# Performance work log

Measured on AMD Instinct MI355X. Metric: run time of the kernel, lower is better.

## Reference

```python
import jax, jax.numpy as jnp
from jax import lax
import numpy as np

CH = 16
STAGES = 6
DN = ('NDHWC', 'DHWIO', 'NDHWC')


def setup_inputs() -> dict:
    key = jax.random.key(0)
    ks = jax.random.split(key, 16)
    B, G = 8, 64
    x = jax.random.normal(ks[0], (B, G, G, G, 1), dtype=jnp.float32)
    mask = jax.random.randint(ks[1], (B, G, G, G), 0, 2, dtype=jnp.int32)
    meta = jax.random.normal(ks[2], (B, 3), dtype=jnp.float32)
    sched = jax.random.normal(ks[3], (B, 128), dtype=jnp.float32)
    s = 0.05
    w_stem = jax.random.normal(ks[4], (5, 5, 5, 1, CH), dtype=jnp.float32) * s
    w_stages = jax.random.normal(ks[5], (STAGES, 3, 3, 3, CH, CH), dtype=jnp.float32) * s
    meta_w1 = jax.random.normal(ks[6], (3, 32), dtype=jnp.float32) * s
    meta_b1 = jnp.zeros((32,), jnp.float32)
    meta_w2 = jax.random.normal(ks[7], (32, 16), dtype=jnp.float32) * s
    meta_b2 = jnp.zeros((16,), jnp.float32)
    mat_w = jax.random.normal(ks[8], (CH * STAGES + 16, 128), dtype=jnp.float32) * s
    mat_b = jnp.zeros((128,), jnp.float32)
    sch_w = jax.random.normal(ks[9], (128, 128), dtype=jnp.float32) * s
    sch_b = jnp.zeros((128,), jnp.float32)
    f1_w = jax.random.normal(ks[10], (256, 128), dtype=jnp.float32) * s
    f1_b = jnp.zeros((128,), jnp.float32)
    f2_w = jax.random.normal(ks[11], (128, 1), dtype=jnp.float32) * s
    f2_b = jnp.zeros((1,), jnp.float32)
    return dict(x=x, mask=mask, meta=meta, sched=sched, w_stem=w_stem,
                w_stages=w_stages, meta_w1=meta_w1, meta_b1=meta_b1,
                meta_w2=meta_w2, meta_b2=meta_b2, mat_w=mat_w, mat_b=mat_b,
                sch_w=sch_w, sch_b=sch_b, f1_w=f1_w, f1_b=f1_b,
                f2_w=f2_w, f2_b=f2_b)


def _pool_mask(m):
    # ME stride-2 output coords = unique(coords // 2): 2x2x2 max-pool, ceil sizes
    return lax.reduce_window(m, jnp.float32(0), lax.max,
                             (1, 2, 2, 2), (1, 2, 2, 2), 'SAME')


def reference(x, mask, meta, sched, w_stem, w_stages, meta_w1, meta_b1,
              meta_w2, meta_b2, mat_w, mat_b, sch_w, sch_b,
              f1_w, f1_b, f2_w, f2_b):
    m = mask.astype(x.dtype)
    feats = x * m[..., None]                       # zero features off-mask
    y = lax.conv_general_dilated(feats, w_stem, (1, 1, 1), 'SAME',
                                 dimension_numbers=DN)
    y = jnp.maximum(y * m[..., None], 0.0)         # stem: conv + mask + ReLU
    pools = []
    for i in range(STAGES):
        y = lax.conv_general_dilated(y, w_stages[i], (2, 2, 2),
                                     [(1, 1), (1, 1), (1, 1)],
                                     dimension_numbers=DN)
        m = _pool_mask(m)
        y = jnp.maximum(y * m[..., None], 0.0)
        denom = jnp.maximum(m.sum(axis=(1, 2, 3)), 1.0)   # occupied voxels
        pools.append(y.sum(axis=(1, 2, 3)) / denom[:, None])
    pools = jnp.concatenate(pools, axis=1)                 # [B, CH*STAGES]
    h = jax.nn.relu(meta[:, :3] @ meta_w1 + meta_b1)
    meta_emb = h @ meta_w2 + meta_b2                        # [B,16]
    m_emb = jax.nn.relu(jnp.concatenate([pools, meta_emb], 1) @ mat_w + mat_b)
    s_emb = jax.nn.relu(sched @ sch_w + sch_b)
    z = jnp.concatenate([m_emb, s_emb], axis=1)             # [B,256]
    z = jax.nn.relu(z @ f1_w + f1_b)
    return z @ f2_w + f2_b                                  # [B,1]
```

## Files before the change

### kernel.cpp

```cpp
#include <hip/hip_runtime.h>

#define CH 16
#define NB 8

typedef unsigned short u16;
typedef unsigned int u32;
typedef __attribute__((ext_vector_type(8))) short s16x8;
typedef __attribute__((ext_vector_type(4))) float f32x4;

__device__ __forceinline__ float bflo(u32 u) { return __uint_as_float(u << 16); }
__device__ __forceinline__ float bfhi(u32 u) { return __uint_as_float(u & 0xffff0000u); }
__device__ __forceinline__ u32 bfrnd(float f) {
  u32 u = __float_as_uint(f);
  return (u + 0x7fffu + ((u >> 16) & 1u)) >> 16;
}
__device__ __forceinline__ u32 packbf_hw(float lo, float hi) {
  u32 r;
  asm("v_cvt_pk_bf16_f32 %0, %1, %2" : "=v"(r) : "v"(lo), "v"(hi));
  return r;
}

__global__ __launch_bounds__(256) void bprep_kernel(
    const float* __restrict__ w_stg, const float* __restrict__ w_stem,
    u16* __restrict__ bpre)
{
  const int e = blockIdx.x * 256 + (int)threadIdx.x;
  if (e >= 4 * 7168 + 3584) return;
  if (e < 4 * 7168) {
    const int s = e / 7168, r0 = e % 7168;
    const int i = r0 >> 9;
    const int r = r0 & 511;
    const int l = r >> 3, j = r & 7;
    const int tap = 2 * i + (l >> 5);
    const int cin = ((l >> 4) & 1) * 8 + j;
    const int n = l & 15;
    const float* w = w_stg + s * 27 * 256;
    const float val = (tap < 27) ? w[(tap * 16 + cin) * 16 + n] : 0.f;
    bpre[s * 7168 + i * 512 + l * 8 + j] = (u16)bfrnd(val);
  } else {
    const int e2 = e - 4 * 7168;
    const int i = e2 >> 9;
    const int r0 = e2 & 511;
    const int lane = r0 >> 3, j = r0 & 7;
    const int quad = lane >> 4, n = lane & 15;
    const int r = i * 4 + quad;
    const float val = (r < 25 && j < 5) ? w_stem[(r * 5 + j) * 16 + n] : 0.f;
    bpre[4 * 7168 + e2] = (u16)bfrnd(val);
  }
}

__global__ __launch_bounds__(256, 6) void stem_mfma(
    const float* __restrict__ x, const int* __restrict__ mask,
    const u16* __restrict__ bpre, u16* __restrict__ yout,
    float* __restrict__ pool_sum, float* __restrict__ cnt)
{
  __shared__ u16 cp[8 * 1168];

  const int b = blockIdx.y;
  const int u = blockIdx.x;
  const int tb = ((u & 7) << 6) | (u >> 3);
  const int z0 = (tb >> 6) * 8;
  const int y0 = ((tb >> 3) & 7) * 8;
  const int x0 = (tb & 7) * 8;
  const int tid = threadIdx.x;

  if (tb == 0) {
    if (tid < 96) pool_sum[b * 96 + tid] = 0.f;
    else if (tid < 102) cnt[b * 6 + (tid - 96)] = 0.f;
  }

  const int lane = tid & 63;
  const int wv = tid >> 6;
  const int n = lane & 15;
  const int quad = lane >> 4;
  const int vy = n >> 2, vx = n & 3;

  s16x8 wf[7];
  {
    const s16x8* wfp = (const s16x8*)(bpre + 4 * 7168);
#pragma unroll
    for (int i = 0; i < 7; ++i) wf[i] = wfp[i * 64 + lane];
  }

  if (tid < 144) {
    const int lz = tid / 12, ly = tid - lz * 12;
    const int gz = z0 + lz - 2, gy = y0 + ly - 2;
    uint4* dst = (uint4*)&cp[tid * 8];
    if ((unsigned)gz < 64u && (unsigned)gy < 64u) {
      const long long rowg =
          ((long long)((b * 64 + gz) * 64 + gy)) * 64 + (x0 - 2);
      float v[12];
      if (rowg >= 0 && rowg + 12 <= (long long)NB * 64 * 64 * 64) {
        const float2* xp = (const float2*)(x + rowg);
        const int2* mp2 = (const int2*)(mask + rowg);
        float2 xv[6]; int2 mv2[6];
#pragma unroll
        for (int j = 0; j < 6; ++j) { xv[j] = xp[j]; mv2[j] = mp2[j]; }
#pragma unroll
        for (int j = 0; j < 6; ++j) {
          v[2 * j]     = xv[j].x * (float)mv2[j].x;
          v[2 * j + 1] = xv[j].y * (float)mv2[j].y;
        }
        if (x0 == 0)  { v[0] = 0.f;  v[1] = 0.f;  }
        if (x0 == 56) { v[10] = 0.f; v[11] = 0.f; }
      } else {
#pragma unroll
        for (int j = 0; j < 12; ++j) {
          const int gx = x0 - 2 + j;
          float vv = 0.f;
          if ((unsigned)gx < 64u) {
            const long long gi = rowg + j;
            vv = x[gi] * (float)mask[gi];
          }
          v[j] = vv;
        }
      }
      const u32 c0 = packbf_hw(v[0], v[1]);
      const u32 c1 = packbf_hw(v[2], v[3]);
      const u32 c2 = packbf_hw(v[4], v[5]);
      const u32 c3 = packbf_hw(v[6], v[7]);
      const u32 c4 = packbf_hw(v[8], v[9]);
      const u32 c5 = packbf_hw(v[10], v[11]);
      const u32 d0 = packbf_hw(v[1], v[2]);
      const u32 d1 = packbf_hw(v[3], v[4]);
      const u32 d2 = packbf_hw(v[5], v[6]);
      const u32 d3 = packbf_hw(v[7], v[8]);
      const u32 d4 = packbf_hw(v[9], v[10]);
      const u32 d5 = packbf_hw(v[11], 0.f);
      dst[0 * 146] = make_uint4(c0, c1, c2, c3);
      dst[1 * 146] = make_uint4(d0, d1, d2, d3);
      dst[2 * 146] = make_uint4(c1, c2, c3, c4);
      dst[3 * 146] = make_uint4(d1, d2, d3, d4);
      dst[4 * 146] = make_uint4(c2, c3, c4, c5);
      dst[5 * 146] = make_uint4(d2, d3, d4, d5);
      dst[6 * 146] = make_uint4(c3, c4, c5, 0u);
      dst[7 * 146] = make_uint4(d3, d4, d5, 0u);
    } else {
#pragma unroll
      for (int p = 0; p < 8; ++p) dst[p * 146] = make_uint4(0u, 0u, 0u, 0u);
    }
  }
  __syncthreads();

  int doff[7];
#pragma unroll
  for (int i = 0; i < 7; ++i) {
    const int r = i * 4 + quad;
    doff[i] = (r < 25) ? ((r / 5) * 12 + (r % 5)) * 8 : 0;
  }
  const int base0 = vx * 1168 + (wv * 12 + vy) * 8;
  const int gi0 = ((b * 64 + z0 + wv) * 64 + y0 + vy) * 64 + x0 + vx;
  u16* outp = yout + (size_t)gi0 * 16 + quad * 4;

  float mvc = (float)mask[gi0];
  for (int s = 0; s < 8; ++s) {
    const int sz = (s >> 2) * 4, sy2 = ((s >> 1) & 1) * 4, sx = (s & 1) * 4;
    const int off = sz * 4096 + sy2 * 64 + sx;
    float mvn = 0.f;
    if (s < 7) {
      const int s1 = s + 1;
      const int offn = ((s1 >> 2) * 4) * 4096 + (((s1 >> 1) & 1) * 4) * 64 +
                       (s1 & 1) * 4;
      mvn = (float)mask[gi0 + offn];
    }
    const int base = base0 + sx * 1168 + (sz * 12 + sy2) * 8;
    f32x4 acc = {0.f, 0.f, 0.f, 0.f};
#pragma unroll
    for (int i = 0; i < 7; ++i) {
      const s16x8 bf = *(const s16x8*)&cp[base + doff[i]];
      acc = __builtin_amdgcn_mfma_f32_16x16x32_bf16(wf[i], bf, acc, 0, 0, 0);
    }
    const float f0 = fmaxf(acc[0], 0.f) * mvc;
    const float f1 = fmaxf(acc[1], 0.f) * mvc;
    const float f2 = fmaxf(acc[2], 0.f) * mvc;
    const float f3 = fmaxf(acc[3], 0.f) * mvc;
    *(uint2*)(outp + (size_t)off * 16) =
        make_uint2(packbf_hw(f0, f1), packbf_hw(f2, f3));
    mvc = mvn;
  }
}

template <int S>
__global__ __launch_bounds__(256) void stage_mfma4(
    const u16* __restrict__ yin, const u16* __restrict__ bpre,
    const int* __restrict__ m_in_i, const float* __restrict__ m_in_f,
    u16* __restrict__ yout, float* __restrict__ m_out,
    float* __restrict__ pool_sum, float* __restrict__ cnt,
    const int stage)
{
  __shared__ u16 lb[14 * 512];
  __shared__ float lC[4 * 16 * 17];
  __shared__ float lmp[256];

  constexpr int So = S >> 1;
  constexpr int nvox = So * So * So;
  const int b = blockIdx.y;
  const int tid = threadIdx.x;
  const int vg0 = blockIdx.x * 256;

  {
    const uint4* src = (const uint4*)bpre;
    uint4* dst = (uint4*)lb;
    for (int e = tid; e < 896; e += 256) dst[e] = src[e];
  }

  {
    const int vox = vg0 + tid;
    const int oz = vox / (So * So);
    const int oy = (vox / So) % So;
    const int ox = vox % So;
    float mp = 0.f;
#pragma unroll
    for (int dz = 0; dz < 2; ++dz)
#pragma unroll
      for (int dy = 0; dy < 2; ++dy)
#pragma unroll
        for (int dx = 0; dx < 2; ++dx) {
          const int mi =
              ((b * S + 2 * oz + dz) * S + 2 * oy + dy) * S + 2 * ox + dx;
          const float mv = m_in_i ? (float)m_in_i[mi] : m_in_f[mi];
          mp = fmaxf(mp, mv);
        }
    lmp[tid] = mp;
  }
  __syncthreads();

  const int wv = tid >> 6;
  const int lane = tid & 63;
  const int m = lane & 15;
  const int quad = lane >> 4;
  const int qh = quad >> 1;
  const int qlo = quad & 1;

  int izb[4], iyb[4], ixb[4];
#pragma unroll
  for (int g = 0; g < 4; ++g) {
    const int vox = vg0 + wv * 64 + g * 16 + m;
    const int oz = vox / (So * So);
    const int oy = (vox / So) % So;
    const int ox = vox % So;
    izb[g] = 2 * oz - 1;
    iyb[g] = 2 * oy - 1;
    ixb[g] = 2 * ox - 1;
  }

  const s16x8* lbv = (const s16x8*)lb;
  f32x4 acc[4];
#pragma unroll
  for (int g = 0; g < 4; ++g) acc[g] = (f32x4){0.f, 0.f, 0.f, 0.f};

#pragma unroll
  for (int i = 0; i < 14; ++i) {
    const int t0 = 2 * i, t1 = 2 * i + 1;
    const int dz0 = t0 / 9, dy0 = (t0 / 3) % 3, dx0 = t0 % 3;
    const int dz1 = (t1 < 27) ? t1 / 9 : 1;
    const int dy1 = (t1 < 27) ? (t1 / 3) % 3 : 1;
    const int dx1 = (t1 < 27) ? t1 % 3 : 1;
    const int dzq = qh ? dz1 : dz0;
    const int dyq = qh ? dy1 : dy0;
    const int dxq = qh ? dx1 : dx0;

    uint4 ar[4];
#pragma unroll
    for (int g = 0; g < 4; ++g) {
      const int iz = izb[g] + dzq;
      const int iy = iyb[g] + dyq;
      const int ix = ixb[g] + dxq;
      const bool valid = (unsigned)iz < (unsigned)S &&
                         (unsigned)iy < (unsigned)S &&
                         (unsigned)ix < (unsigned)S;
      const int izc = min(max(iz, 0), S - 1);
      const int iyc = min(max(iy, 0), S - 1);
      const int ixc = min(max(ix, 0), S - 1);
      const size_t addr =
          (size_t)(((b * S + izc) * S + iyc) * S + ixc) * 16 + qlo * 8;
      uint4 v = *(const uint4*)(yin + addr);
      v.x = valid ? v.x : 0u;
      v.y = valid ? v.y : 0u;
      v.z = valid ? v.z : 0u;
      v.w = valid ? v.w : 0u;
      ar[g] = v;
    }
    const s16x8 bfrag = lbv[i * 64 + lane];
#pragma unroll
    for (int g = 0; g < 4; ++g)
      acc[g] = __builtin_amdgcn_mfma_f32_16x16x32_bf16(
          __builtin_bit_cast(s16x8, ar[g]), bfrag, acc[g], 0, 0, 0);
  }

  float psum = 0.f;
#pragma unroll
  for (int g = 0; g < 4; ++g) {
    __syncthreads();
    {
      float* lCw = lC + wv * 272;
      const int n = lane & 15;
#pragma unroll
      for (int reg = 0; reg < 4; ++reg) {
        const int row = quad * 4 + reg;
        lCw[row * 17 + n] =
            fmaxf(acc[g][reg], 0.f) * lmp[wv * 64 + g * 16 + row];
      }
    }
    __syncthreads();
    {
      const int vox_l = tid >> 2;
      const int cg = (tid & 3) * 4;
      const float* src = lC + (vox_l >> 4) * 272 + (vox_l & 15) * 17 + cg;
      const float f0 = src[0], f1 = src[1], f2 = src[2], f3 = src[3];
      const int lv = (vox_l >> 4) * 64 + g * 16 + (vox_l & 15);
      const size_t gi = (size_t)b * nvox + vg0 + lv;
      uint2* op = (uint2*)(yout + gi * 16 + cg);
      op[0] = make_uint2(packbf_hw(f0, f1), packbf_hw(f2, f3));
      if ((tid & 3) == 0) m_out[gi] = lmp[lv];
    }
    if (tid < 16) {
      float s = 0.f;
#pragma unroll 16
      for (int v = 0; v < 64; ++v)
        s += lC[(v >> 4) * 272 + (v & 15) * 17 + tid];
      psum += s;
    }
  }
  if (tid < 16) {
    atomicAdd(&pool_sum[(b * 6 + stage) * 16 + tid], psum);
  } else if (tid == 16) {
    float c = 0.f;
#pragma unroll 16
    for (int v = 0; v < 256; ++v) c += lmp[v];
    atomicAdd(&cnt[b * 6 + stage], c);
  }
}

__global__ __launch_bounds__(256) void tail_kernel(
    const u16* __restrict__ y3g, const float* __restrict__ m3g,
    const u16* __restrict__ bpre,
    const float* __restrict__ wstg,
    const float* __restrict__ meta, const float* __restrict__ sched,
    const float* __restrict__ mw1, const float* __restrict__ mb1,
    const float* __restrict__ mw2, const float* __restrict__ mb2,
    const float* __restrict__ matw, const float* __restrict__ matb,
    const float* __restrict__ schw, const float* __restrict__ schb,
    const float* __restrict__ f1w, const float* __restrict__ f1b,
    const float* __restrict__ f2w, const float* __restrict__ f2b,
    const float* __restrict__ pool_sum, const float* __restrict__ cnt,
    float* __restrict__ out)
{
  const int b = blockIdx.x;
  const int t = threadIdx.x;
  __shared__ u16 ty3[8192];
  __shared__ float lm3[512];
  __shared__ float pb[4 * 64 * 17];
  __shared__ float ly4[64 * 16];
  __shared__ float lm4[64];
  __shared__ float ps4[256];
  __shared__ float ly5[8 * 16];
  __shared__ float lm5[8];
  __shared__ float ps5[128];
  __shared__ float lsum[3][16];
  __shared__ float lcnt[3];
  __shared__ float invec[112];
  __shared__ float hbuf[32];
  __shared__ float zbuf[256];
  __shared__ float psf[256];
  __shared__ float part[2];

  {
    const uint4* yb = (const uint4*)(y3g + (size_t)b * 8192);
    uint4* dst = (uint4*)ty3;
    for (int i = t; i < 1024; i += 256) dst[i] = yb[i];
    for (int i = t; i < 512; i += 256) lm3[i] = m3g[b * 512 + i];
  }
  __syncthreads();

  {
    const int lane = t & 63;
    const int wv = t >> 6;
    const int mm = lane & 15;
    const int quad = lane >> 4;
    const int qh = quad >> 1, qlo = quad & 1;

    int iz0[4], iy0[4], ix0[4];
#pragma unroll
    for (int g = 0; g < 4; ++g) {
      const int vox = g * 16 + mm;
      iz0[g] = 2 * (vox >> 4) - 1;
      iy0[g] = 2 * ((vox >> 2) & 3) - 1;
      ix0[g] = 2 * (vox & 3) - 1;
    }
    f32x4 a3[4];
#pragma unroll
    for (int g = 0; g < 4; ++g) a3[g] = (f32x4){0.f, 0.f, 0.f, 0.f};
    const s16x8* bp3 = (const s16x8*)(bpre + 3 * 7168);
#pragma unroll
    for (int ii = 0; ii < 4; ++ii) {
      const int i = wv * 4 + ii;
      if (i < 14) {
        const int t0 = 2 * i, t1 = 2 * i + 1;
        const int dz0 = t0 / 9, dy0 = (t0 / 3) % 3, dx0 = t0 % 3;
        const int dz1 = (t1 < 27) ? t1 / 9 : 1;
        const int dy1 = (t1 < 27) ? (t1 / 3) % 3 : 1;
        const int dx1 = (t1 < 27) ? t1 % 3 : 1;
        const int dzq = qh ? dz1 : dz0;
        const int dyq = qh ? dy1 : dy0;
        const int dxq = qh ? dx1 : dx0;
        uint4 ar[4];
#pragma unroll
        for (int g = 0; g < 4; ++g) {
          const int iz = iz0[g] + dzq;
          const int iy = iy0[g] + dyq;
          const int ix = ix0[g] + dxq;
          const bool valid = (unsigned)iz < 8u && (unsigned)iy < 8u &&
                             (unsigned)ix < 8u;
          const int izc = min(max(iz, 0), 7);
          const int iyc = min(max(iy, 0), 7);
          const int ixc = min(max(ix, 0), 7);
          const int ad = ((izc * 8 + iyc) * 8 + ixc) * 16 + qlo * 8;
          uint4 v = *(const uint4*)&ty3[ad];
          v.x = valid ? v.x : 0u;
          v.y = valid ? v.y : 0u;
          v.z = valid ? v.z : 0u;
          v.w = valid ? v.w : 0u;
          ar[g] = v;
        }
        const s16x8 bf = bp3[i * 64 + lane];
#pragma unroll
        for (int g = 0; g < 4; ++g)
          a3[g] = __builtin_amdgcn_mfma_f32_16x16x32_bf16(
              __builtin_bit_cast(s16x8, ar[g]), bf, a3[g], 0, 0, 0);
      }
    }
#pragma unroll
    for (int g = 0; g < 4; ++g)
#pragma unroll
      for (int reg = 0; reg < 4; ++reg)
        pb[wv * 1088 + (g * 16 + quad * 4 + reg) * 17 + mm] = a3[g][reg];
  }
  __syncthreads();

  {
    const int vox = t >> 2, cg = (t & 3) * 4;
    const int oz = vox >> 4, oy = (vox >> 2) & 3, ox = vox & 3;
    float mp = 0.f;
#pragma unroll
    for (int dz = 0; dz < 2; ++dz)
#pragma unroll
      for (int dy = 0; dy < 2; ++dy)
#pragma unroll
        for (int dx = 0; dx < 2; ++dx)
          mp = fmaxf(mp, lm3[((2 * oz + dz) * 8 + 2 * oy + dy) * 8 +
                             2 * ox + dx]);
#pragma unroll
    for (int c = 0; c < 4; ++c) {
      const int ch = cg + c;
      const float s = pb[vox * 17 + ch] + pb[1088 + vox * 17 + ch] +
                      pb[2176 + vox * 17 + ch] + pb[3264 + vox * 17 + ch];
      ly4[vox * 16 + ch] = fmaxf(s, 0.f) * mp;
    }
    if (cg == 0) lm4[vox] = mp;
  }
  __syncthreads();

  if (t < 16) {
    float s = 0.f;
#pragma unroll 16
    for (int v = 0; v < 64; ++v) s += ly4[v * 16 + t];
    lsum[0][t] = s;
  } else if (t == 16) {
    float s = 0.f;
#pragma unroll 16
    for (int v = 0; v < 64; ++v) s += lm4[v];
    lcnt[0] = s;
  }
  {
    const float* w = wstg + 4 * 27 * 256;
    const int o = t >> 1, kh = t & 1;
    const int vox4 = o >> 4, co = o & 15;
    const int oz = vox4 >> 2, oy = (vox4 >> 1) & 1, ox = vox4 & 1;
    float acc = 0.f;
#pragma unroll
    for (int tt = 0; tt < 14; ++tt) {
      const int tap = tt + (kh ? 14 : 0);
      if (tap < 27) {
        const int dz = tap / 9, dy = (tap / 3) % 3, dx = tap % 3;
        const int iz = 2 * oz + dz - 1, iy = 2 * oy + dy - 1,
                  ix = 2 * ox + dx - 1;
        const float s = ((unsigned)iz < 4u && (unsigned)iy < 4u &&
                         (unsigned)ix < 4u) ? 1.f : 0.f;
        const int idx = ((min(max(iz, 0), 3) * 4 + min(max(iy, 0), 3)) * 4 +
                         min(max(ix, 0), 3)) * 16;
        const float* wp = w + tap * 256 + co;
#pragma unroll
        for (int ci = 0; ci < 16; ++ci)
          acc = fmaf(ly4[idx + ci] * s, wp[ci * 16], acc);
      }
    }
    ps4[t] = acc;
  }
  __syncthreads();

  if (t < 128) {
    const int vox4 = t >> 4, co = t & 15;
    float mp = 0.f;
#pragma unroll
    for (int dz = 0; dz < 2; ++dz)
#pragma unroll
      for (int dy = 0; dy < 2; ++dy)
#pragma unroll
        for (int dx = 0; dx < 2; ++dx)
          mp = fmaxf(mp, lm4[((2 * (vox4 >> 2) + dz) * 4 +
                              2 * ((vox4 >> 1) & 1) + dy) * 4 +
                             2 * (vox4 & 1) + dx]);
    ly5[t] = fmaxf(ps4[2 * t] + ps4[2 * t + 1], 0.f) * mp;
    if (co == 0) lm5[vox4] = mp;
  }
  __syncthreads();

  if (t < 16) {
    float s = 0.f;
#pragma unroll
    for (int v = 0; v < 8; ++v) s += ly5[v * 16 + t];
    lsum[1][t] = s;
  } else if (t == 16) {
    lcnt[1] = lm5[0] + lm5[1] + lm5[2] + lm5[3] + lm5[4] + lm5[5] + lm5[6] +
              lm5[7];
  }
  if (t < 128) {
    const float* w = wstg + 5 * 27 * 256;
    const int co = t & 15, k8 = t >> 4;
    float acc = 0.f;
#pragma unroll
    for (int tt = 0; tt < 4; ++tt) {
      const int tap = k8 * 4 + tt;
      if (tap < 27) {
        const int dz = tap / 9, dy = (tap / 3) % 3, dx = tap % 3;
        const int iz = dz - 1, iy = dy - 1, ix = dx - 1;
        const float s = ((unsigned)iz < 2u && (unsigned)iy < 2u &&
                         (unsigned)ix < 2u) ? 1.f : 0.f;
        const int idx = ((min(max(iz, 0), 1) * 2 + min(max(iy, 0), 1)) * 2 +
                         min(max(ix, 0), 1)) * 16;
        const float* wp = w + tap * 256 + co;
#pragma unroll
        for (int ci = 0; ci < 16; ++ci)
          acc = fmaf(ly5[idx + ci] * s, wp[ci * 16], acc);
      }
    }
    ps5[t] = acc;
  }
  __syncthreads();

  if (t < 16) {
    float s = ps5[t] + ps5[16 + t] + ps5[32 + t] + ps5[48 + t] +
              ps5[64 + t] + ps5[80 + t] + ps5[96 + t] + ps5[112 + t];
    float mp = 0.f;
#pragma unroll
    for (int v = 0; v < 8; ++v) mp = fmaxf(mp, lm5[v]);
    lsum[2][t] = fmaxf(s, 0.f) * mp;
    if (t == 0) lcnt[2] = mp;
  } else if (t >= 96 && t < 128) {
    const int j = t - 96;
    float h = mb1[j];
#pragma unroll
    for (int k = 0; k < 3; ++k) h = fmaf(meta[b * 3 + k], mw1[k * 32 + j], h);
    hbuf[j] = fmaxf(h, 0.f);
  }
  __syncthreads();

  if (t < 48) {
    const int s = t >> 4;
    invec[t] = pool_sum[b * 96 + t] / fmaxf(cnt[b * 6 + s], 1.f);
  } else if (t < 96) {
    const int s = (t >> 4) - 3;
    invec[t] = lsum[s][t & 15] / fmaxf(lcnt[s], 1.f);
  } else if (t < 112) {
    const int j = t - 96;
    float e = mb2[j];
#pragma unroll
    for (int k = 0; k < 32; ++k) e = fmaf(hbuf[k], mw2[k * 16 + j], e);
    invec[t] = e;
  }
  __syncthreads();

  if (t < 128) {
    float a = matb[t];
#pragma unroll 16
    for (int k = 0; k < 112; ++k) a = fmaf(invec[k], matw[k * 128 + t], a);
    zbuf[t] = fmaxf(a, 0.f);
  } else {
    const int c = t - 128;
    float s = schb[c];
#pragma unroll 16
    for (int k = 0; k < 128; ++k)
      s = fmaf(sched[b * 128 + k], schw[k * 128 + c], s);
    zbuf[128 + c] = fmaxf(s, 0.f);
  }
  __syncthreads();

  {
    const int col = t & 127, kh = t >> 7;
    float a = 0.f;
#pragma unroll 16
    for (int kk = 0; kk < 128; ++kk) {
      const int k = kh * 128 + kk;
      a = fmaf(zbuf[k], f1w[k * 128 + col], a);
    }
    psf[t] = a;
  }
  __syncthreads();

  if (t < 128) {
    const float a = psf[t] + psf[128 + t] + f1b[t];
    float v = fmaxf(a, 0.f) * f2w[t];
#pragma unroll
    for (int off = 32; off > 0; off >>= 1) v += __shfl_xor(v, off, 64);
    if ((t & 63) == 0) part[t >> 6] = v;
  }
  __syncthreads();
  if (t == 0) out[b] = part[0] + part[1] + f2b[0];
}

extern "C" void kernel_launch(void* const* d_in, const int* in_sizes, int n_in,
                              void* d_out, int out_size, void* d_ws,
                              size_t ws_size, hipStream_t stream)
{
  (void)in_sizes; (void)n_in; (void)out_size; (void)ws_size;
  const float* x      = (const float*)d_in[0];
  const int*   mask   = (const int*)  d_in[1];
  const float* meta   = (const float*)d_in[2];
  const float* sched  = (const float*)d_in[3];
  const float* w_stem = (const float*)d_in[4];
  const float* w_stg  = (const float*)d_in[5];
  const float* mw1    = (const float*)d_in[6];
  const float* mb1    = (const float*)d_in[7];
  const float* mw2    = (const float*)d_in[8];
  const float* mb2    = (const float*)d_in[9];
  const float* matw   = (const float*)d_in[10];
  const float* matb   = (const float*)d_in[11];
  const float* schw   = (const float*)d_in[12];
  const float* schb   = (const float*)d_in[13];
  const float* f1w    = (const float*)d_in[14];
  const float* f1b    = (const float*)d_in[15];
  const float* f2w    = (const float*)d_in[16];
  const float* f2b    = (const float*)d_in[17];
  float* out = (float*)d_out;

  char* ws = (char*)d_ws;
  size_t off = 0;
  auto alloc = [&](size_t nbytes) -> void* {
    void* p = ws + off;
    off += (nbytes + 255) & ~(size_t)255;
    return p;
  };

  u16* y0 = (u16*)alloc((size_t)NB * 64 * 64 * 64 * CH * 2);
  u16* y1 = (u16*)alloc((size_t)NB * 32 * 32 * 32 * CH * 2);
  u16* y2 = (u16*)alloc((size_t)NB * 16 * 16 * 16 * CH * 2);
  u16* y3 = (u16*)alloc((size_t)NB * 8 * 8 * 8 * CH * 2);
  float* m1 = (float*)alloc((size_t)NB * 32 * 32 * 32 * 4);
  float* m2 = (float*)alloc((size_t)NB * 16 * 16 * 16 * 4);
  float* m3 = (float*)alloc((size_t)NB * 8 * 8 * 8 * 4);
  float* pool_sum = (float*)alloc((NB * 96 + NB * 6) * 4);
  float* cnt = pool_sum + NB * 96;
  u16* bpre = (u16*)alloc((4 * 7168 + 3584) * 2);

  bprep_kernel<<<126, 256, 0, stream>>>(w_stg, w_stem, bpre);

  stem_mfma<<<dim3(512, NB), 256, 0, stream>>>(x, mask, bpre, y0,
                                               pool_sum, cnt);

  stage_mfma4<64><<<dim3(128, NB), 256, 0, stream>>>(
      y0, bpre + 0 * 7168, mask, (const float*)nullptr, y1, m1,
      pool_sum, cnt, 0);
  stage_mfma4<32><<<dim3(16, NB), 256, 0, stream>>>(
      y1, bpre + 1 * 7168, (const int*)nullptr, m1, y2, m2,
      pool_sum, cnt, 1);
  stage_mfma4<16><<<dim3(2, NB), 256, 0, stream>>>(
      y2, bpre + 2 * 7168, (const int*)nullptr, m2, y3, m3,
      pool_sum, cnt, 2);

  tail_kernel<<<NB, 256, 0, stream>>>(y3, m3, bpre, w_stg, meta, sched,
                                      mw1, mb1, mw2, mb2, matw, matb,
                                      schw, schb, f1w, f1b, f2w, f2b,
                                      pool_sum, cnt, out);
}
```

Before: 196.5 us.

## Split stem MFMA accumulators, store masks as bytes, remap stage block order

The stem loop now alternates its MFMAs between two accumulators and sums them at the end, which shortens the dependent MFMA chain. Intermediate pooled masks are stored as u8 instead of float, cutting mask write and read traffic between stages. Stage-0 blocks are remapped so consecutive block IDs spread across the volume, which may change cache or channel locality. These are independent ideas, and they cost a few extra registers and adds.

```diff
diff --git a/kernel.cpp b/kernel.cpp
--- a/kernel.cpp
+++ b/kernel.cpp
@@ -4,6 +4,7 @@
 #define NB 8
 
 typedef unsigned short u16;
+typedef unsigned char u8;
 typedef unsigned int u32;
 typedef __attribute__((ext_vector_type(8))) short s16x8;
 typedef __attribute__((ext_vector_type(4))) float f32x4;
@@ -164,16 +165,20 @@
       mvn = (float)mask[gi0 + offn];
     }
     const int base = base0 + sx * 1168 + (sz * 12 + sy2) * 8;
-    f32x4 acc = {0.f, 0.f, 0.f, 0.f};
+    f32x4 accA = {0.f, 0.f, 0.f, 0.f};
+    f32x4 accB = {0.f, 0.f, 0.f, 0.f};
 #pragma unroll
     for (int i = 0; i < 7; ++i) {
       const s16x8 bf = *(const s16x8*)&cp[base + doff[i]];
-      acc = __builtin_amdgcn_mfma_f32_16x16x32_bf16(wf[i], bf, acc, 0, 0, 0);
-    }
-    const float f0 = fmaxf(acc[0], 0.f) * mvc;
-    const float f1 = fmaxf(acc[1], 0.f) * mvc;
-    const float f2 = fmaxf(acc[2], 0.f) * mvc;
-    const float f3 = fmaxf(acc[3], 0.f) * mvc;
+      if (i & 1)
+        accB = __builtin_amdgcn_mfma_f32_16x16x32_bf16(wf[i], bf, accB, 0, 0, 0);
+      else
+        accA = __builtin_amdgcn_mfma_f32_16x16x32_bf16(wf[i], bf, accA, 0, 0, 0);
+    }
+    const float f0 = fmaxf(accA[0] + accB[0], 0.f) * mvc;
+    const float f1 = fmaxf(accA[1] + accB[1], 0.f) * mvc;
+    const float f2 = fmaxf(accA[2] + accB[2], 0.f) * mvc;
+    const float f3 = fmaxf(accA[3] + accB[3], 0.f) * mvc;
     *(uint2*)(outp + (size_t)off * 16) =
         make_uint2(packbf_hw(f0, f1), packbf_hw(f2, f3));
     mvc = mvn;
@@ -183,8 +188,8 @@
 template <int S>
 __global__ __launch_bounds__(256) void stage_mfma4(
     const u16* __restrict__ yin, const u16* __restrict__ bpre,
-    const int* __restrict__ m_in_i, const float* __restrict__ m_in_f,
-    u16* __restrict__ yout, float* __restrict__ m_out,
+    const int* __restrict__ m_in_i, const u8* __restrict__ m_in_u8,
+    u16* __restrict__ yout, u8* __restrict__ m_out,
     float* __restrict__ pool_sum, float* __restrict__ cnt,
     const int stage)
 {
@@ -194,9 +199,14 @@
 
   constexpr int So = S >> 1;
   constexpr int nvox = So * So * So;
+  constexpr int NBX = nvox / 256;
   const int b = blockIdx.y;
   const int tid = threadIdx.x;
-  const int vg0 = blockIdx.x * 256;
+  const int u = blockIdx.x;
+  int bxi;
+  if constexpr (NBX >= 8) bxi = (u & 7) * (NBX / 8) + (u >> 3);
+  else bxi = u;
+  const int vg0 = bxi * 256;
 
   {
     const uint4* src = (const uint4*)bpre;
@@ -218,7 +228,7 @@
         for (int dx = 0; dx < 2; ++dx) {
           const int mi =
               ((b * S + 2 * oz + dz) * S + 2 * oy + dy) * S + 2 * ox + dx;
-          const float mv = m_in_i ? (float)m_in_i[mi] : m_in_f[mi];
+          const float mv = m_in_i ? (float)m_in_i[mi] : (float)m_in_u8[mi];
           mp = fmaxf(mp, mv);
         }
     lmp[tid] = mp;
@@ -312,7 +322,7 @@
       const size_t gi = (size_t)b * nvox + vg0 + lv;
       uint2* op = (uint2*)(yout + gi * 16 + cg);
       op[0] = make_uint2(packbf_hw(f0, f1), packbf_hw(f2, f3));
-      if ((tid & 3) == 0) m_out[gi] = lmp[lv];
+      if ((tid & 3) == 0) m_out[gi] = (u8)lmp[lv];
     }
     if (tid < 16) {
       float s = 0.f;
@@ -333,7 +343,7 @@
 }
 
 __global__ __launch_bounds__(256) void tail_kernel(
-    const u16* __restrict__ y3g, const float* __restrict__ m3g,
+    const u16* __restrict__ y3g, const u8* __restrict__ m3g,
     const u16* __restrict__ bpre,
     const float* __restrict__ wstg,
     const float* __restrict__ meta, const float* __restrict__ sched,
@@ -369,7 +379,7 @@
     const uint4* yb = (const uint4*)(y3g + (size_t)b * 8192);
     uint4* dst = (uint4*)ty3;
     for (int i = t; i < 1024; i += 256) dst[i] = yb[i];
-    for (int i = t; i < 512; i += 256) lm3[i] = m3g[b * 512 + i];
+    for (int i = t; i < 512; i += 256) lm3[i] = (float)m3g[b * 512 + i];
   }
   __syncthreads();
 
@@ -656,9 +666,9 @@
   u16* y1 = (u16*)alloc((size_t)NB * 32 * 32 * 32 * CH * 2);
   u16* y2 = (u16*)alloc((size_t)NB * 16 * 16 * 16 * CH * 2);
   u16* y3 = (u16*)alloc((size_t)NB * 8 * 8 * 8 * CH * 2);
-  float* m1 = (float*)alloc((size_t)NB * 32 * 32 * 32 * 4);
-  float* m2 = (float*)alloc((size_t)NB * 16 * 16 * 16 * 4);
-  float* m3 = (float*)alloc((size_t)NB * 8 * 8 * 8 * 4);
+  u8* m1 = (u8*)alloc((size_t)NB * 32 * 32 * 32);
+  u8* m2 = (u8*)alloc((size_t)NB * 16 * 16 * 16);
+  u8* m3 = (u8*)alloc((size_t)NB * 8 * 8 * 8);
   float* pool_sum = (float*)alloc((NB * 96 + NB * 6) * 4);
   float* cnt = pool_sum + NB * 96;
   u16* bpre = (u16*)alloc((4 * 7168 + 3584) * 2);
@@ -669,7 +679,7 @@
                                                pool_sum, cnt);
 
   stage_mfma4<64><<<dim3(128, NB), 256, 0, stream>>>(
-      y0, bpre + 0 * 7168, mask, (const float*)nullptr, y1, m1,
+      y0, bpre + 0 * 7168, mask, (const u8*)nullptr, y1, m1,
       pool_sum, cnt, 0);
   stage_mfma4<32><<<dim3(16, NB), 256, 0, stream>>>(
       y1, bpre + 1 * 7168, (const int*)nullptr, m1, y2, m2,
```

Result: no change. 196.8 us (+0.1%).
